# Kernel tuning notes

Hardware: AMD Instinct MI355X
Metric: run time of the kernel (lower is better)

## Reference

```python
import jax, jax.numpy as jnp
import numpy as np

B, S, H = 2, 2048, 1024
NH, DH = 16, 64  # num heads, head dim

def setup_inputs() -> dict:
    key = jax.random.key(0)
    ks = jax.random.split(key, 4)
    scale = 0.02
    return {
        "hidden_states": jax.random.normal(ks[0], (B, S, H), dtype=jnp.float32),
        "attention_mask": jnp.zeros((B, 1, 1, S), dtype=jnp.float32),  # additive mask
        "Wq": jax.random.normal(ks[1], (H, H), dtype=jnp.float32) * scale,
        "bq": jnp.zeros((H,), dtype=jnp.float32),
        "Wk": jax.random.normal(ks[2], (H, H), dtype=jnp.float32) * scale,
        "bk": jnp.zeros((H,), dtype=jnp.float32),
        "Wv": jax.random.normal(ks[3], (H, H), dtype=jnp.float32) * scale,
        "bv": jnp.zeros((H,), dtype=jnp.float32),
    }

def _split_heads(x):
    # [B,S,H] -> [B,NH,S,DH]
    return x.reshape(B, S, NH, DH).transpose(0, 2, 1, 3)

def reference(hidden_states, attention_mask, Wq, bq, Wk, bk, Wv, bv):
    q = _split_heads(hidden_states @ Wq + bq)
    k = _split_heads(hidden_states @ Wk + bk)
    v = _split_heads(hidden_states @ Wv + bv)
    # scores: [B,NH,S,S]
    scores = jnp.einsum('bhqd,bhkd->bhqk', q, k) / jnp.asarray(np.sqrt(DH), scores_dtype := q.dtype)
    scores = scores + attention_mask  # additive mask broadcast
    probs = jax.nn.softmax(scores, axis=-1)
    out = jnp.einsum('bhqk,bhkd->bhqd', probs, v)  # [B,NH,S,DH]
    out = out.transpose(0, 2, 1, 3).reshape(B, S, H)
    return out
```

## Files before the change

### kernel.cpp

```cpp
#include <hip/hip_runtime.h>
#include <hip/hip_bf16.h>

#define Bn  2
#define Sn  2048
#define Hn  1024
#define NHn 16
#define DHn 64
#define Mn  (Bn * Sn)

typedef __attribute__((ext_vector_type(4)))  float    f32x4;
typedef __attribute__((ext_vector_type(16))) float    f32x16;
typedef __attribute__((ext_vector_type(8)))  _Float16 h8;
typedef __attribute__((ext_vector_type(4)))  _Float16 h4;
typedef __attribute__((ext_vector_type(2)))  __fp16   fp16x2;
typedef __attribute__((ext_vector_type(2)))  unsigned int u32x2;

union H2PK { fp16x2 v; unsigned int u; };
union U4H8 { unsigned int u[4]; h8 v; };

#define MFMA16F(a, b, c) __builtin_amdgcn_mfma_f32_16x16x32_f16(a, b, c, 0, 0, 0)
#define MFMA32F(a, b, c) __builtin_amdgcn_mfma_f32_32x32x16_f16(a, b, c, 0, 0, 0)

#define SCFULL 0.18033688011112042f
#define L2E    1.44269504088896340736f

__device__ __forceinline__ void glds16(const void* g, void* l) {
    __builtin_amdgcn_global_load_lds(
        (const __attribute__((address_space(1))) unsigned int*)g,
        (__attribute__((address_space(3))) unsigned int*)l, 16, 0, 0);
}

__global__ __launch_bounds__(256) void prep(
    const float* __restrict__ X, const float* __restrict__ W0,
    const float* __restrict__ W1, const float* __restrict__ W2,
    const float* __restrict__ Msk,
    _Float16* __restrict__ Xh, _Float16* __restrict__ WT,
    _Float16* __restrict__ Wm)
{
    const int bid = blockIdx.x;
    const int tid = threadIdx.x;
    __shared__ float Ws[64][65];

    if (bid < 4096) {
        const int i = bid * 256 + tid;
        float4 x = ((const float4*)X)[i];
        h4 o;
        o[0] = (_Float16)x.x; o[1] = (_Float16)x.y;
        o[2] = (_Float16)x.z; o[3] = (_Float16)x.w;
        *(h4*)&Xh[(size_t)i * 4] = o;
        return;
    }
    if (bid >= 4096 + 768) {
#pragma unroll
        for (int it = 0; it < 16; ++it) {
            const int idx = it * 256 + tid;
            Wm[idx] = (_Float16)__builtin_amdgcn_exp2f(Msk[idx] * L2E);
        }
        return;
    }

    const int wb = bid - 4096;
    const int which = wb >> 8;
    const int rem = wb & 255;
    const int k0 = ((rem >> 4) & 15) * 64;
    const int n0 = (rem & 15) * 64;
    const float* W = (which == 0) ? W0 : (which == 1 ? W1 : W2);
    _Float16* O = WT + (size_t)which * Hn * Hn;

#pragma unroll
    for (int it = 0; it < 4; ++it) {
        const int idx = tid + 256 * it;
        const int row = idx >> 4, c4 = (idx & 15) * 4;
        float4 w = *(const float4*)&W[(size_t)(k0 + row) * Hn + n0 + c4];
        Ws[row][c4 + 0] = w.x; Ws[row][c4 + 1] = w.y;
        Ws[row][c4 + 2] = w.z; Ws[row][c4 + 3] = w.w;
    }
    __syncthreads();
#pragma unroll
    for (int it = 0; it < 16; ++it) {
        const int e = tid + 256 * it;
        const int k = e & 63, n = e >> 6;
        O[(size_t)(n0 + n) * Hn + k0 + k] = (_Float16)Ws[k][n];
    }
}

__global__ __launch_bounds__(256) void qkv_mfma(
    const _Float16* __restrict__ Xh, const _Float16* __restrict__ WTA,
    const float* __restrict__ b0, const float* __restrict__ b1,
    const float* __restrict__ b2, const _Float16* __restrict__ Wm,
    _Float16* __restrict__ Qh, _Float16* __restrict__ Kh,
    _Float16* __restrict__ VTh)
{
    const int which = blockIdx.z;
    const _Float16* WT = WTA + (size_t)which * Hn * Hn;
    const float* bias = (which == 0) ? b0 : (which == 1 ? b1 : b2);
    _Float16* Dst = (which == 0) ? Qh : (which == 1 ? Kh : VTh);

    const int m0 = blockIdx.x * 128;
    const int n0 = blockIdx.y * 128;
    const int tid  = threadIdx.x;
    const int wid  = tid >> 6;
    const int lane = tid & 63;
    const int l16  = lane & 15;
    const int quad = lane >> 4;
    const int wm = wid >> 1, wn = wid & 1;

    __shared__ _Float16 Ah[128 * 64], Bh[128 * 64];

    f32x4 acc[4][4];
#pragma unroll
    for (int i = 0; i < 4; ++i)
#pragma unroll
        for (int j = 0; j < 4; ++j) acc[i][j] = (f32x4){0.f, 0.f, 0.f, 0.f};

    for (int kt = 0; kt < Hn / 64; ++kt) {
        const int k0 = kt * 64;
        __syncthreads();
#pragma unroll
        for (int c = 0; c < 4; ++c) {
            const int idx = (wid * 4 + c) * 64 + lane;
            const int row = idx >> 3;
            const int cg  = (idx & 7) ^ (row & 7);
            glds16(&Xh[(size_t)(m0 + row) * Hn + k0 + cg * 8],
                   &Ah[(wid * 4 + c) * 512]);
            glds16(&WT[(size_t)(n0 + row) * Hn + k0 + cg * 8],
                   &Bh[(wid * 4 + c) * 512]);
        }
        __syncthreads();

#pragma unroll
        for (int kk = 0; kk < 2; ++kk) {
            h8 xa[4], wb[4];
#pragma unroll
            for (int t = 0; t < 4; ++t) {
                const int ar = wm * 64 + t * 16 + l16;
                const int br = wn * 64 + t * 16 + l16;
                xa[t] = *(const h8*)&Ah[ar * 64 + (((kk * 4 + quad) ^ (ar & 7)) * 8)];
                wb[t] = *(const h8*)&Bh[br * 64 + (((kk * 4 + quad) ^ (br & 7)) * 8)];
            }
            if (which < 2) {
#pragma unroll
                for (int i = 0; i < 4; ++i)
#pragma unroll
                    for (int j = 0; j < 4; ++j)
                        acc[i][j] = MFMA16F(xa[i], wb[j], acc[i][j]);
            } else {
#pragma unroll
                for (int i = 0; i < 4; ++i)
#pragma unroll
                    for (int j = 0; j < 4; ++j)
                        acc[i][j] = MFMA16F(wb[i], xa[j], acc[i][j]);
            }
        }
    }

    const float oscale = (which == 0) ? SCFULL : 1.0f;
    if (which < 2) {
#pragma unroll
        for (int j = 0; j < 4; ++j) {
            const int n = n0 + wn * 64 + j * 16 + l16;
            const float bv = bias[n];
            const int hh = n >> 6, dd = n & 63;
#pragma unroll
            for (int i = 0; i < 4; ++i) {
                const int mb = m0 + wm * 64 + i * 16 + quad * 4;
#pragma unroll
                for (int r = 0; r < 4; ++r) {
                    const int m = mb + r;
                    const int b = m >> 11, s = m & (Sn - 1);
                    Dst[(((size_t)b * NHn + hh) * Sn + s) * DHn + dd] =
                        (_Float16)((acc[i][j][r] + bv) * oscale);
                }
            }
        }
    } else {
        float wvj[4];
#pragma unroll
        for (int j = 0; j < 4; ++j)
            wvj[j] = (float)Wm[m0 + wm * 64 + j * 16 + l16];
#pragma unroll
        for (int i = 0; i < 4; ++i) {
#pragma unroll
            for (int r = 0; r < 4; ++r) {
                const int n = n0 + wn * 64 + i * 16 + quad * 4 + r;
                const float bv = bias[n];
                const int hh = n >> 6, dd = n & 63;
#pragma unroll
                for (int j = 0; j < 4; ++j) {
                    const int m = m0 + wm * 64 + j * 16 + l16;
                    const int b = m >> 11, s = m & (Sn - 1);
                    Dst[(((size_t)b * NHn + hh) * DHn + dd) * Sn + s] =
                        (_Float16)((acc[i][j][r] + bv) * wvj[j]);
                }
            }
        }
    }
}

__global__ __launch_bounds__(256, 3) void attn(
    const _Float16* __restrict__ Qh, const _Float16* __restrict__ Kh,
    const _Float16* __restrict__ VTh, const _Float16* __restrict__ Wmg,
    float* __restrict__ Out)
{
    const int flat = blockIdx.x + 32 * blockIdx.y + 512 * blockIdx.z;
    const int bh   = ((flat & 7) << 2) | ((flat >> 3) & 3);
    const int qb   = flat >> 5;
    const int b = bh >> 4, h = bh & 15;

    const int tid  = threadIdx.x;
    const int wid  = tid >> 6;
    const int lane = tid & 63;
    const int l32  = lane & 31;
    const int hi   = lane >> 5;
    const int qsub = wid & 1;
    const int kh   = wid >> 1;

    __shared__ __align__(16) _Float16 Kb[3][4096];
    __shared__ __align__(16) _Float16 Vb[3][4096];
    __shared__ __align__(16) _Float16 Wb[3][512];

    const int q0 = qb * 64 + qsub * 32;

    const size_t qbase = ((size_t)bh * Sn + q0 + l32) * DHn;
    h8 qf[4];
#pragma unroll
    for (int kd = 0; kd < 4; ++kd)
        qf[kd] = *(const h8*)&Qh[qbase + kd * 16 + hi * 8];

    asm volatile("s_waitcnt vmcnt(0)" ::: "memory");

    const _Float16* Kg = Kh  + (size_t)bh * Sn * DHn;
    const _Float16* Vg = VTh + (size_t)bh * DHn * Sn;
    const _Float16* Wg = Wmg + (size_t)b * Sn;

    auto stage = [&](int kt, int buf) {
        const int koff = kt * 64;
#pragma unroll
        for (int c = 0; c < 2; ++c) {
            const int idx = (wid * 2 + c) * 64 + lane;
            const int row = idx >> 3;
            const int cg  = (idx & 7) ^ (row & 7);
            glds16(&Kg[(size_t)(koff + row) * DHn + cg * 8],
                   &Kb[buf][(wid * 2 + c) * 512]);
            glds16(&Vg[(size_t)row * Sn + koff + cg * 8],
                   &Vb[buf][(wid * 2 + c) * 512]);
        }
        glds16(&Wg[koff + lane * 8], &Wb[buf][0]);
    };

    stage(0, 0);
    stage(1, 1);

    f32x16 sA, sB, o[2], acc_l;
#pragma unroll
    for (int dt = 0; dt < 2; ++dt) o[dt] = (f32x16)(0.f);
    acc_l = (f32x16)(0.f);

    auto qkt = [&](f32x16& s, int buf) {
        __builtin_amdgcn_s_setprio(1);
        f32x16 c = (f32x16)(0.f);
#pragma unroll
        for (int kd = 0; kd < 4; ++kd) {
            const int row = kh * 32 + l32;
            h8 kf = *(const h8*)&Kb[buf][row * 64 +
                                         (((kd * 2 + hi) ^ (row & 7)) * 8)];
            c = MFMA32F(kf, qf[kd], c);
        }
        s = c;
        __builtin_amdgcn_s_setprio(0);
    };

    auto sm_pv = [&](f32x16& s, int buf) {
        unsigned int pk[4][2];
#pragma unroll
        for (int g = 0; g < 4; ++g) {
            const float p0 = __builtin_amdgcn_exp2f(s[g * 4 + 0]);
            const float p1 = __builtin_amdgcn_exp2f(s[g * 4 + 1]);
            const float p2 = __builtin_amdgcn_exp2f(s[g * 4 + 2]);
            const float p3 = __builtin_amdgcn_exp2f(s[g * 4 + 3]);
            H2PK u0, u1;
            u0.v = __builtin_amdgcn_cvt_pkrtz(p0, p1);
            u1.v = __builtin_amdgcn_cvt_pkrtz(p2, p3);
            pk[g][0] = u0.u;
            pk[g][1] = u1.u;
        }

        __builtin_amdgcn_s_setprio(1);
#pragma unroll
        for (int ks = 0; ks < 2; ++ks) {
            const int ge = ks * 2;
            u32x2 rA = __builtin_amdgcn_permlane32_swap(
                pk[ge][0], pk[ge + 1][0], false, false);
            u32x2 rB = __builtin_amdgcn_permlane32_swap(
                pk[ge][1], pk[ge + 1][1], false, false);
            U4H8 w;
            w.u[0] = rA[0]; w.u[1] = rB[0]; w.u[2] = rA[1]; w.u[3] = rB[1];
            h8 wv8 = *(const h8*)&Wb[buf][kh * 32 + ks * 16 + hi * 8];
            acc_l = MFMA32F(w.v, wv8, acc_l);
#pragma unroll
            for (int dt = 0; dt < 2; ++dt) {
                const int row = dt * 32 + l32;
                h8 vf = *(const h8*)&Vb[buf][row * 64 +
                           (((kh * 4 + ks * 2 + hi) ^ (row & 7)) * 8)];
                o[dt] = MFMA32F(w.v, vf, o[dt]);
            }
        }
        __builtin_amdgcn_s_setprio(0);
    };

    asm volatile("s_waitcnt vmcnt(5)" ::: "memory");
    __builtin_amdgcn_s_barrier();
    asm volatile("" ::: "memory");
    qkt(sA, 0);

    int bc = 0, bn = 1, bs = 2;
    auto iter = [&](int kt, f32x16& scur, f32x16& snxt) {
        asm volatile("s_waitcnt vmcnt(0)" ::: "memory");
        __builtin_amdgcn_s_barrier();
        asm volatile("" ::: "memory");
        if (kt + 2 < Sn / 64) stage(kt + 2, bs);
        qkt(snxt, bn);
        sm_pv(scur, bc);
        const int t = bc; bc = bn; bn = bs; bs = t;
    };

    for (int kt = 0; kt < 30; kt += 2) {
        iter(kt,     sA, sB);
        iter(kt + 1, sB, sA);
    }
    asm volatile("s_waitcnt vmcnt(0)" ::: "memory");
    __builtin_amdgcn_s_barrier();
    asm volatile("" ::: "memory");
    qkt(sB, bn);
    sm_pv(sA, bc);
    sm_pv(sB, bn);

    __syncthreads();
    float* scr = (float*)&Kb[0][0];
    if (wid >= 2) {
        float* p = scr + ((size_t)(wid - 2) * 64 + lane) * 48;
#pragma unroll
        for (int i = 0; i < 16; ++i) p[i]      = o[0][i];
#pragma unroll
        for (int i = 0; i < 16; ++i) p[16 + i] = o[1][i];
#pragma unroll
        for (int i = 0; i < 16; ++i) p[32 + i] = acc_l[i];
    }
    __syncthreads();
    if (wid < 2) {
        const float* p = scr + ((size_t)qsub * 64 + lane) * 48;
#pragma unroll
        for (int g2 = 0; g2 < 4; ++g2) {
#pragma unroll
            for (int e = 0; e < 4; ++e) {
                const int r = g2 * 4 + e;
                const int q = q0 + 4 * hi + 8 * g2 + e;
                const size_t ob = ((size_t)b * Sn + q) * Hn + h * DHn;
                const float sc = 1.0f / (acc_l[r] + p[32 + r]);
#pragma unroll
                for (int dt = 0; dt < 2; ++dt)
                    Out[ob + dt * 32 + l32] = (o[dt][r] + p[dt * 16 + r]) * sc;
            }
        }
    }
}

extern "C" void kernel_launch(void* const* d_in, const int* in_sizes, int n_in,
                              void* d_out, int out_size, void* d_ws, size_t ws_size,
                              hipStream_t stream) {
    const float* X    = (const float*)d_in[0];
    const float* mask = (const float*)d_in[1];
    const float* Wq   = (const float*)d_in[2];
    const float* bq   = (const float*)d_in[3];
    const float* Wk   = (const float*)d_in[4];
    const float* bk   = (const float*)d_in[5];
    const float* Wv   = (const float*)d_in[6];
    const float* bv   = (const float*)d_in[7];
    float* out = (float*)d_out;

    const size_t NE = (size_t)Mn * Hn;
    _Float16* Xh  = (_Float16*)d_ws;
    _Float16* WT  = Xh + NE;
    _Float16* Qh  = WT + (size_t)3 * Hn * Hn;
    _Float16* Kh  = Qh + NE;
    _Float16* VTh = Kh + NE;
    _Float16* Wm  = VTh + NE;

    prep<<<dim3(4096 + 768 + 1), dim3(256), 0, stream>>>(
        X, Wq, Wk, Wv, mask, Xh, WT, Wm);

    dim3 g1(Mn / 128, Hn / 128, 3), b1(256);
    qkv_mfma<<<g1, b1, 0, stream>>>(Xh, WT, bq, bk, bv, Wm, Qh, Kh, VTh);

    dim3 g2(Sn / 64, NHn, Bn), b2(256);
    attn<<<g2, b2, 0, stream>>>(Qh, Kh, VTh, Wm, out);
}
```

Baseline: 177.9 us.

## Widen attention blocks to 128 queries with 4-stage K/V ring buffer

The attention kernel now runs 512-thread blocks covering 128 query rows, so each staged K/V/mask tile is shared by twice as many waves and the block count halves. The 3-buffer rotation becomes a 4-buffer ring indexed by kt&3. Each tile's load is issued before the barrier with a partial vmcnt wait, which lets the next load overlap the current compute. The reduction scratch stride is padded from 48 to 49 floats to avoid LDS bank conflicts. The risk is that launch bounds of (512,4) force a tight VGPR budget that may cause spills, and larger LDS use per block limits how many blocks are resident.

```diff
diff --git a/kernel.cpp b/kernel.cpp
--- a/kernel.cpp
+++ b/kernel.cpp
@@ -197,12 +197,12 @@
     }
 }
 
-__global__ __launch_bounds__(256, 3) void attn(
+__global__ __launch_bounds__(512, 4) void attn(
     const _Float16* __restrict__ Qh, const _Float16* __restrict__ Kh,
     const _Float16* __restrict__ VTh, const _Float16* __restrict__ Wmg,
     float* __restrict__ Out)
 {
-    const int flat = blockIdx.x + 32 * blockIdx.y + 512 * blockIdx.z;
+    const int flat = blockIdx.x + 16 * blockIdx.y + 256 * blockIdx.z;
     const int bh   = ((flat & 7) << 2) | ((flat >> 3) & 3);
     const int qb   = flat >> 5;
     const int b = bh >> 4, h = bh & 15;
@@ -212,14 +212,15 @@
     const int lane = tid & 63;
     const int l32  = lane & 31;
     const int hi   = lane >> 5;
-    const int qsub = wid & 1;
-    const int kh   = wid >> 1;
-
-    __shared__ __align__(16) _Float16 Kb[3][4096];
-    __shared__ __align__(16) _Float16 Vb[3][4096];
-    __shared__ __align__(16) _Float16 Wb[3][512];
-
-    const int q0 = qb * 64 + qsub * 32;
+    const int qsub = wid >> 1;
+    const int kh   = wid & 1;
+
+    __shared__ __align__(16) _Float16 smem[4 * 4096 + 4 * 4096 + 4 * 512];
+    _Float16* Kb = smem;
+    _Float16* Vb = smem + 16384;
+    _Float16* Wb = smem + 32768;
+
+    const int q0 = qb * 128 + qsub * 32;
 
     const size_t qbase = ((size_t)bh * Sn + q0 + l32) * DHn;
     h8 qf[4];
@@ -235,17 +236,14 @@
 
     auto stage = [&](int kt, int buf) {
         const int koff = kt * 64;
-#pragma unroll
-        for (int c = 0; c < 2; ++c) {
-            const int idx = (wid * 2 + c) * 64 + lane;
-            const int row = idx >> 3;
-            const int cg  = (idx & 7) ^ (row & 7);
-            glds16(&Kg[(size_t)(koff + row) * DHn + cg * 8],
-                   &Kb[buf][(wid * 2 + c) * 512]);
-            glds16(&Vg[(size_t)row * Sn + koff + cg * 8],
-                   &Vb[buf][(wid * 2 + c) * 512]);
-        }
-        glds16(&Wg[koff + lane * 8], &Wb[buf][0]);
+        const int idx = wid * 64 + lane;
+        const int row = idx >> 3;
+        const int cg  = (idx & 7) ^ (row & 7);
+        glds16(&Kg[(size_t)(koff + row) * DHn + cg * 8],
+               &Kb[buf * 4096 + wid * 512]);
+        glds16(&Vg[(size_t)row * Sn + koff + cg * 8],
+               &Vb[buf * 4096 + wid * 512]);
+        glds16(&Wg[koff + lane * 8], &Wb[buf * 512]);
     };
 
     stage(0, 0);
@@ -262,8 +260,8 @@
 #pragma unroll
         for (int kd = 0; kd < 4; ++kd) {
             const int row = kh * 32 + l32;
-            h8 kf = *(const h8*)&Kb[buf][row * 64 +
-                                         (((kd * 2 + hi) ^ (row & 7)) * 8)];
+            h8 kf = *(const h8*)&Kb[buf * 4096 + row * 64 +
+                                    (((kd * 2 + hi) ^ (row & 7)) * 8)];
             c = MFMA32F(kf, qf[kd], c);
         }
         s = c;
@@ -295,12 +293,12 @@
                 pk[ge][1], pk[ge + 1][1], false, false);
             U4H8 w;
             w.u[0] = rA[0]; w.u[1] = rB[0]; w.u[2] = rA[1]; w.u[3] = rB[1];
-            h8 wv8 = *(const h8*)&Wb[buf][kh * 32 + ks * 16 + hi * 8];
+            h8 wv8 = *(const h8*)&Wb[buf * 512 + kh * 32 + ks * 16 + hi * 8];
             acc_l = MFMA32F(w.v, wv8, acc_l);
 #pragma unroll
             for (int dt = 0; dt < 2; ++dt) {
                 const int row = dt * 32 + l32;
-                h8 vf = *(const h8*)&Vb[buf][row * 64 +
+                h8 vf = *(const h8*)&Vb[buf * 4096 + row * 64 +
                            (((kh * 4 + ks * 2 + hi) ^ (row & 7)) * 8)];
                 o[dt] = MFMA32F(w.v, vf, o[dt]);
             }
@@ -308,20 +306,18 @@
         __builtin_amdgcn_s_setprio(0);
     };
 
-    asm volatile("s_waitcnt vmcnt(5)" ::: "memory");
+    asm volatile("s_waitcnt vmcnt(3)" ::: "memory");
     __builtin_amdgcn_s_barrier();
     asm volatile("" ::: "memory");
     qkt(sA, 0);
 
-    int bc = 0, bn = 1, bs = 2;
     auto iter = [&](int kt, f32x16& scur, f32x16& snxt) {
-        asm volatile("s_waitcnt vmcnt(0)" ::: "memory");
+        stage(kt + 2, (kt + 2) & 3);
+        asm volatile("s_waitcnt vmcnt(3)" ::: "memory");
         __builtin_amdgcn_s_barrier();
         asm volatile("" ::: "memory");
-        if (kt + 2 < Sn / 64) stage(kt + 2, bs);
-        qkt(snxt, bn);
-        sm_pv(scur, bc);
-        const int t = bc; bc = bn; bn = bs; bs = t;
+        qkt(snxt, (kt + 1) & 3);
+        sm_pv(scur, kt & 3);
     };
 
     for (int kt = 0; kt < 30; kt += 2) {
@@ -331,14 +327,14 @@
     asm volatile("s_waitcnt vmcnt(0)" ::: "memory");
     __builtin_amdgcn_s_barrier();
     asm volatile("" ::: "memory");
-    qkt(sB, bn);
-    sm_pv(sA, bc);
-    sm_pv(sB, bn);
+    qkt(sB, 31 & 3);
+    sm_pv(sA, 30 & 3);
+    sm_pv(sB, 31 & 3);
 
     __syncthreads();
-    float* scr = (float*)&Kb[0][0];
-    if (wid >= 2) {
-        float* p = scr + ((size_t)(wid - 2) * 64 + lane) * 48;
+    float* scr = (float*)smem;
+    if (kh == 1) {
+        float* p = scr + ((size_t)qsub * 64 + lane) * 49;
 #pragma unroll
         for (int i = 0; i < 16; ++i) p[i]      = o[0][i];
 #pragma unroll
@@ -347,8 +343,8 @@
         for (int i = 0; i < 16; ++i) p[32 + i] = acc_l[i];
     }
     __syncthreads();
-    if (wid < 2) {
-        const float* p = scr + ((size_t)qsub * 64 + lane) * 48;
+    if (kh == 0) {
+        const float* p = scr + ((size_t)qsub * 64 + lane) * 49;
 #pragma unroll
         for (int g2 = 0; g2 < 4; ++g2) {
 #pragma unroll
@@ -392,6 +388,6 @@
     dim3 g1(Mn / 128, Hn / 128, 3), b1(256);
     qkv_mfma<<<g1, b1, 0, stream>>>(Xh, WT, bq, bk, bv, Wm, Qh, Kh, VTh);
 
-    dim3 g2(Sn / 64, NHn, Bn), b2(256);
+    dim3 g2(Sn / 128, NHn, Bn), b2(512);
     attn<<<g2, b2, 0, stream>>>(Qh, Kh, VTh, Wm, out);
 }
```

Measured after the change: 172.0 us. -3.3%, faster.
